# Kernel optimization log

Hardware: AMD Instinct MI355X
Metric: run time of the kernel (lower is better)

Reference implementation:

```python
import jax, jax.numpy as jnp
import numpy as np
import math

DIM = 512
MIN_THRES = -5.0
MAX_THRES = 7.0


def setup_inputs() -> dict:
    key = jax.random.key(0)
    k1, k2, k3, k4, k5 = jax.random.split(key, 5)
    s_len, batch, dim = 256, 256, DIM
    x = jax.random.normal(k1, (s_len, batch, dim), dtype=jnp.float32)
    # Linear(dim, dim, bias=False) weights, torch convention y = x @ W.T
    Wq = jax.random.normal(k2, (dim, dim), dtype=jnp.float32) * 0.02
    Wk = jax.random.normal(k3, (dim, dim), dtype=jnp.float32) * 0.02
    Wv = jax.random.normal(k4, (dim, dim), dtype=jnp.float32) * 0.02
    root_query = jax.random.normal(k5, (dim,), dtype=jnp.float32)
    return {"x": x, "Wq": Wq, "Wk": Wk, "Wv": Wv, "root_query": root_query}


def _matrix_tree(score):
    # score: [b, s, s]. Batched matrix-tree theorem marginals (lengths=None -> full length).
    b, s, _ = score.shape
    eye = jnp.eye(s, dtype=score.dtype)
    A = jnp.exp(score)                                  # exp(input)
    rd = jnp.exp(jnp.diagonal(score, axis1=1, axis2=2))  # exp(diag) root scores [b, s]
    L_off = A * (1.0 - eye)                              # mask diagonal
    colsum = L_off.sum(axis=1)                           # lap.sum(0): column sums [b, s]
    lap = -L_off + eye * colsum[:, None, :]              # -A_off + diag(colsum)
    lap = lap.at[:, 0, :].set(rd)                        # lap[0] = exp(diag(input))
    inv = jnp.linalg.inv(lap)                            # [b, s, s]
    inv_diag = jnp.diagonal(inv, axis1=1, axis2=2)       # [b, s]
    term1 = A * inv_diag[:, None, :]                     # factor[i,j] = inv_diag[j]
    term2 = A * jnp.swapaxes(inv, 1, 2)
    term1 = term1.at[:, :, 0].set(0.0)
    term2 = term2.at[:, 0, :].set(0.0)
    roots = rd * inv[:, :, 0]                            # diag(input).exp() * inv.T[0]
    return term1 - term2 + roots[:, :, None] * eye       # [b, s, s]


def reference(x, Wq, Wk, Wv, root_query):
    s_len, batch, dim = x.shape
    scale = math.sqrt(1.0 / dim)
    xt = jnp.swapaxes(x, 0, 1)                           # [b, s, d]
    q = jnp.einsum('bsd,ed->bse', xt, Wq)
    k = jnp.einsum('bsd,ed->bse', xt, Wk)
    v = jnp.einsum('bsd,ed->bse', xt, Wv)
    _score = jnp.einsum('bsd,btd->bst', q, k)            # [b, s, s]
    root = jnp.einsum('bsd,d->bs', k, root_query)        # [b, s]
    eye = jnp.eye(s_len, dtype=x.dtype)
    # Faithful to source: score[b] = _score[b]*eye + diag(root[b]) (off-diagonal zeroed)
    score = _score * eye + root[:, :, None] * eye
    score = jnp.clip(score * scale, MIN_THRES, MAX_THRES)
    edge_score = jnp.swapaxes(_matrix_tree(score), 1, 2)  # [b, s, s]
    return jnp.einsum('bst,btd->bsd', edge_score, v)
```

## Files before the change

kernel.cpp:

```cpp
#include <hip/hip_runtime.h>

typedef __bf16 v8bf __attribute__((ext_vector_type(8)));
typedef float f32x4 __attribute__((ext_vector_type(4)));
typedef unsigned short u16x8 __attribute__((ext_vector_type(8)));

#define SLEN 256
#define BATCH 256
#define DIM 512
#define SCALE 0.044194173824159216f

#define TS 64
#define LDX 520
#define LDB 72
#define KC 64

#define MFMA(a, b, c) __builtin_amdgcn_mfma_f32_16x16x32_bf16((a), (b), (c), 0, 0, 0)

__device__ __forceinline__ unsigned int f2bf(float f) {
  union { float f; unsigned int u; } v; v.f = f;
  unsigned int r = v.u + 0x7FFFu + ((v.u >> 16) & 1u);
  return r >> 16;
}
__device__ __forceinline__ float bf2f(unsigned short u) {
  union { unsigned int u; float f; } v; v.u = ((unsigned int)u) << 16;
  return v.f;
}
__device__ __forceinline__ v8bf ld8(const unsigned short* p) {
  u16x8 t = *reinterpret_cast<const u16x8*>(p);
  return __builtin_bit_cast(v8bf, t);
}
__device__ __forceinline__ void gload16(const unsigned short* g, unsigned short* l) {
  __builtin_amdgcn_global_load_lds(
      (const __attribute__((address_space(1))) unsigned int*)g,
      (__attribute__((address_space(3))) unsigned int*)l, 16, 0, 0);
}

__global__ __launch_bounds__(256) void zf(float4* __restrict__ p, int n4) {
  const int i = blockIdx.x * 256 + threadIdx.x;
  if (i < n4) {
    const float4 z = {0.f, 0.f, 0.f, 0.f};
    p[i] = z;
  }
}

__global__ __launch_bounds__(256) void prep_all(const float* __restrict__ X,
                                                const float* __restrict__ Wq,
                                                const float* __restrict__ Wk,
                                                const float* __restrict__ Wv,
                                                const float* __restrict__ rq,
                                                unsigned short* __restrict__ Xsb,
                                                unsigned short* __restrict__ Mt,
                                                unsigned short* __restrict__ Wvb,
                                                float* __restrict__ wkr) {
  __shared__ float As[32][33];
  __shared__ float Bs[32][33];
  const int blk = blockIdx.x;
  const int tid = threadIdx.x;

  if (blk >= 514) {
    const size_t base = (size_t)(blk - 514) * 16384;
#pragma unroll
    for (int j = 0; j < 8; ++j) {
      const float* s = X + base + (size_t)j * 2048 + tid * 8;
      const float4 a = *reinterpret_cast<const float4*>(s);
      const float4 b = *reinterpret_cast<const float4*>(s + 4);
      uint4 p;
      p.x = f2bf(a.x) | (f2bf(a.y) << 16);
      p.y = f2bf(a.z) | (f2bf(a.w) << 16);
      p.z = f2bf(b.x) | (f2bf(b.y) << 16);
      p.w = f2bf(b.z) | (f2bf(b.w) << 16);
      *reinterpret_cast<uint4*>(Xsb + base + (size_t)j * 2048 + tid * 8) = p;
    }
  } else if (blk < 256) {
    const int e0 = (blk & 15) * 32;
    const int d0 = (blk >> 4) * 32;
    const int tm = (tid & 15) * 2;
    const int tn = (tid >> 4) * 2;
    const int lf = tid >> 3;
    const int lc = (tid & 7) * 4;
    float a00 = 0.f, a01 = 0.f, a10 = 0.f, a11 = 0.f;
    for (int f0 = 0; f0 < DIM; f0 += 32) {
      __syncthreads();
      const float4 a = *reinterpret_cast<const float4*>(Wk + (size_t)(f0 + lf) * DIM + e0 + lc);
      const float4 b = *reinterpret_cast<const float4*>(Wq + (size_t)(f0 + lf) * DIM + d0 + lc);
      As[lf][lc] = a.x; As[lf][lc + 1] = a.y; As[lf][lc + 2] = a.z; As[lf][lc + 3] = a.w;
      Bs[lf][lc] = b.x; Bs[lf][lc + 1] = b.y; Bs[lf][lc + 2] = b.z; Bs[lf][lc + 3] = b.w;
      __syncthreads();
#pragma unroll
      for (int k = 0; k < 32; ++k) {
        const float x0 = As[k][tm], x1 = As[k][tm + 1];
        const float y0 = Bs[k][tn], y1 = Bs[k][tn + 1];
        a00 += x0 * y0; a01 += x0 * y1; a10 += x1 * y0; a11 += x1 * y1;
      }
    }
    Mt[(size_t)(e0 + tm) * DIM + d0 + tn] = (unsigned short)f2bf(a00);
    Mt[(size_t)(e0 + tm) * DIM + d0 + tn + 1] = (unsigned short)f2bf(a01);
    Mt[(size_t)(e0 + tm + 1) * DIM + d0 + tn] = (unsigned short)f2bf(a10);
    Mt[(size_t)(e0 + tm + 1) * DIM + d0 + tn + 1] = (unsigned short)f2bf(a11);
  } else if (blk < 512) {
    const int idx = ((blk - 256) * 256 + tid) * 4;
    const float4 v = *reinterpret_cast<const float4*>(Wv + idx);
    uint2 p;
    p.x = f2bf(v.x) | (f2bf(v.y) << 16);
    p.y = f2bf(v.z) | (f2bf(v.w) << 16);
    *reinterpret_cast<uint2*>(Wvb + idx) = p;
  } else {
    float* rqs = &As[0][0];
    rqs[tid] = rq[tid];
    rqs[tid + 256] = rq[tid + 256];
    __syncthreads();
    const int d = (blk - 512) * 256 + tid;
    float s = 0.f;
#pragma unroll 8
    for (int f = 0; f < DIM; ++f) s += Wk[(size_t)f * DIM + d] * rqs[f];
    wkr[d] = s;
  }
}


#define GEMM_PROLOGUE()                                                         \
  f32x4 acc[8][4] = {};                                                         \
  STG(0); STG(1); STG(2);

#define GEMM_MAIN_LOOP()                                                        \
  for (int t = 0; t < 16; ++t) {                                                \
    if (t <= 13) { asm volatile("s_waitcnt vmcnt(8)" ::: "memory"); }           \
    else if (t == 14) { asm volatile("s_waitcnt vmcnt(4)" ::: "memory"); }      \
    else { asm volatile("s_waitcnt vmcnt(0)" ::: "memory"); }                   \
    __builtin_amdgcn_s_barrier();                                               \
    __builtin_amdgcn_sched_barrier(0);                                          \
    if (t + 3 < 16) { STG(t + 3); }                                             \
    __builtin_amdgcn_sched_barrier(0);                                          \
    const unsigned short* la = lds + (t & 3) * 16384;                           \
    const unsigned short* lb2 = la + 8192;                                      \
    v8bf a[8], bbf[4];                                                          \
    _Pragma("unroll")                                                           \
    for (int m = 0; m < 8; ++m)                                                 \
      a[m] = ld8(la + (wr * 128 + m * 16 + c) * 32 + grd);                      \
    _Pragma("unroll")                                                           \
    for (int n = 0; n < 4; ++n)                                                 \
      bbf[n] = ld8(lb2 + (wc * 64 + n * 16 + c) * 32 + grd);                    \
    __builtin_amdgcn_s_setprio(1);                                              \
    _Pragma("unroll")                                                           \
    for (int m = 0; m < 8; ++m)                                                 \
      _Pragma("unroll")                                                         \
      for (int n = 0; n < 4; ++n) acc[m][n] = MFMA(a[m], bbf[n], acc[m][n]);    \
    __builtin_amdgcn_s_setprio(0);                                              \
  }

#define STG(tt) {                                                               \
    const int kc_ = (tt) * 32;                                                  \
    unsigned short* lb_ = lw + ((tt) & 3) * 16384;                              \
    gload16(sAp + kc_, lb_);                                                    \
    gload16(sAp + kc_ + sA2, lb_ + 4096);                                       \
    gload16(sBp + kc_, lb_ + 8192);                                             \
    gload16(sBp + kc_ + sB2, lb_ + 12288); }

__global__ __launch_bounds__(512, 2) void gemm1_dp(const unsigned short* __restrict__ Xsb,
                                                   const unsigned short* __restrict__ Mt,
                                                   const float* __restrict__ wkr,
                                                   float* __restrict__ rdpart) {
  __shared__ unsigned short lds[65536];
  const int tid = threadIdx.x;
  const int lane = tid & 63, w = tid >> 6;
  const int wr = w >> 2, wc = w & 3;
  const int c = lane & 15, g = lane >> 4;
  const int grd = ((g ^ ((c >> 1) & 3))) * 8;

  const int work = (blockIdx.x & 7) * 64 + (blockIdx.x >> 3);
  const int rt = work >> 1, ct = work & 1;
  const int j0 = rt * 256, e0 = ct * 256;

  const int rA = tid >> 2;
  const int gl = (tid & 3) ^ ((rA >> 1) & 3);
  const unsigned short* sAp = Xsb + ((size_t)rA * BATCH + rt) * DIM + gl * 8;
  const unsigned short* sBp = Mt + (size_t)(e0 + rA) * DIM + gl * 8;
  const size_t sA2 = (size_t)128 * BATCH * DIM;
  const size_t sB2 = (size_t)128 * DIM;
  unsigned short* lw = lds + (w << 9);

  GEMM_PROLOGUE()
  GEMM_MAIN_LOOP()

  __syncthreads();
  float* red = (float*)lds;
  float wkrl[4];
#pragma unroll
  for (int n = 0; n < 4; ++n) wkrl[n] = wkr[e0 + wc * 64 + n * 16 + c];
#pragma unroll
  for (int m = 0; m < 8; ++m) {
#pragma unroll
    for (int i = 0; i < 4; ++i) {
      const int rl = wr * 128 + m * 16 + 4 * g + i;
      const unsigned short* xrow = Xsb + ((size_t)rl * BATCH + rt) * DIM + e0 + wc * 64 + c;
      float val = 0.f;
#pragma unroll
      for (int n = 0; n < 4; ++n)
        val += (acc[m][n][i] + wkrl[n]) * bf2f(xrow[n * 16]);
      val += __shfl_xor(val, 1); val += __shfl_xor(val, 2);
      val += __shfl_xor(val, 4); val += __shfl_xor(val, 8);
      if (c == 0) red[wc * 256 + rl] = val;
    }
  }
  __syncthreads();
  if (tid < 256) {
    const float s = red[tid] + red[256 + tid] + red[512 + tid] + red[768 + tid];
    rdpart[(size_t)ct * 65536 + j0 + tid] = s;
  }
}

__global__ __launch_bounds__(512, 2) void gemm2_f(const unsigned short* __restrict__ Xsb,
                                                  const unsigned short* __restrict__ Wvb,
                                                  const float* __restrict__ rdpart,
                                                  float* __restrict__ out) {
  __shared__ unsigned short lds[65536];
  __shared__ float rdl[256];
  __shared__ float wsum[4];
  const int tid = threadIdx.x;
  const int lane = tid & 63, w = tid >> 6;
  const int wr = w >> 2, wc = w & 3;
  const int c = lane & 15, g = lane >> 4;
  const int grd = ((g ^ ((c >> 1) & 3))) * 8;

  const int work = (blockIdx.x & 7) * 64 + (blockIdx.x >> 3);
  const int rt = work >> 1, ct = work & 1;
  const int j0 = rt * 256, e0 = ct * 256;
  const int b = rt;

  if (tid < 256) {
    float v = (rdpart[(size_t)b * SLEN + tid] + rdpart[65536 + (size_t)b * SLEN + tid]) * SCALE;
    v = fminf(fmaxf(v, -5.0f), 7.0f);
    const float r = expf(v);
    rdl[tid] = r;
    float t = r;
    t += __shfl_xor(t, 1);  t += __shfl_xor(t, 2);  t += __shfl_xor(t, 4);
    t += __shfl_xor(t, 8);  t += __shfl_xor(t, 16); t += __shfl_xor(t, 32);
    if ((tid & 63) == 0) wsum[tid >> 6] = t;
  }
  __syncthreads();

  const int rA = tid >> 2;
  const int gl = (tid & 3) ^ ((rA >> 1) & 3);
  const unsigned short* sAp = Xsb + ((size_t)rA * BATCH + b) * DIM + gl * 8;
  const unsigned short* sBp = Wvb + (size_t)(e0 + rA) * DIM + gl * 8;
  const size_t sA2 = (size_t)128 * BATCH * DIM;
  const size_t sB2 = (size_t)128 * DIM;
  unsigned short* lw = lds + (w << 9);

  GEMM_PROLOGUE()
  GEMM_MAIN_LOOP()

  float vsp[4] = {0.f, 0.f, 0.f, 0.f}, vwp[4] = {0.f, 0.f, 0.f, 0.f};
#pragma unroll
  for (int m = 0; m < 8; ++m) {
#pragma unroll
    for (int i = 0; i < 4; ++i) {
      const int rl = wr * 128 + m * 16 + 4 * g + i;
      const float rr = rdl[rl];
#pragma unroll
      for (int n = 0; n < 4; ++n) {
        vsp[n] += acc[m][n][i];
        vwp[n] += rr * acc[m][n][i];
      }
    }
  }
#pragma unroll
  for (int n = 0; n < 4; ++n) {
    vsp[n] += __shfl_xor(vsp[n], 16); vsp[n] += __shfl_xor(vsp[n], 32);
    vwp[n] += __shfl_xor(vwp[n], 16); vwp[n] += __shfl_xor(vwp[n], 32);
  }
  __syncthreads();
  float* red = (float*)lds;
  if (g == 0) {
#pragma unroll
    for (int n = 0; n < 4; ++n) {
      red[(w * 4 + n) * 16 + c] = vsp[n];
      red[512 + (w * 4 + n) * 16 + c] = vwp[n];
    }
  }
  __syncthreads();
  const float Rb = wsum[0] + wsum[1] + wsum[2] + wsum[3];
  const float invR = 1.0f / Rb;
  const float gam = invR * 0.00390625f;
  const int wo = w ^ 4;
  float vsf[4], vwf[4];
#pragma unroll
  for (int n = 0; n < 4; ++n) {
    vsf[n] = red[(w * 4 + n) * 16 + c] + red[(wo * 4 + n) * 16 + c];
    vwf[n] = red[512 + (w * 4 + n) * 16 + c] + red[512 + (wo * 4 + n) * 16 + c];
  }
#pragma unroll
  for (int m = 0; m < 8; ++m) {
#pragma unroll
    for (int i = 0; i < 4; ++i) {
      const int rl = wr * 128 + m * 16 + 4 * g + i;
      const float tt = rdl[rl] * invR;
      const float al = tt - 0.00390625f;
      const float be = (1.0f - tt) * 0.00390625f;
      float* orow = out + (size_t)(j0 + rl) * DIM + e0 + wc * 64 + c;
#pragma unroll
      for (int n = 0; n < 4; ++n)
        orow[n * 16] = al * acc[m][n][i] + be * vsf[n] + gam * vwf[n];
    }
  }
}

__global__ __launch_bounds__(256) void prep_mt(const float* __restrict__ Wq,
                                               const float* __restrict__ Wk,
                                               unsigned short* __restrict__ Mt) {
  __shared__ float As[32][33];
  __shared__ float Bs[32][33];
  const int e0 = (blockIdx.x & 15) * 32;
  const int d0 = (blockIdx.x >> 4) * 32;
  const int tid = threadIdx.x;
  const int tm = (tid & 15) * 2;
  const int tn = (tid >> 4) * 2;
  const int lf = tid >> 3;
  const int lc = (tid & 7) * 4;
  float a00 = 0.f, a01 = 0.f, a10 = 0.f, a11 = 0.f;
  for (int f0 = 0; f0 < DIM; f0 += 32) {
    __syncthreads();
    const float4 a = *reinterpret_cast<const float4*>(Wk + (size_t)(f0 + lf) * DIM + e0 + lc);
    const float4 b = *reinterpret_cast<const float4*>(Wq + (size_t)(f0 + lf) * DIM + d0 + lc);
    As[lf][lc] = a.x; As[lf][lc + 1] = a.y; As[lf][lc + 2] = a.z; As[lf][lc + 3] = a.w;
    Bs[lf][lc] = b.x; Bs[lf][lc + 1] = b.y; Bs[lf][lc + 2] = b.z; Bs[lf][lc + 3] = b.w;
    __syncthreads();
#pragma unroll
    for (int k = 0; k < 32; ++k) {
      const float x0 = As[k][tm], x1 = As[k][tm + 1];
      const float y0 = Bs[k][tn], y1 = Bs[k][tn + 1];
      a00 += x0 * y0; a01 += x0 * y1; a10 += x1 * y0; a11 += x1 * y1;
    }
  }
  Mt[(size_t)(e0 + tm) * DIM + d0 + tn] = (unsigned short)f2bf(a00);
  Mt[(size_t)(e0 + tm) * DIM + d0 + tn + 1] = (unsigned short)f2bf(a01);
  Mt[(size_t)(e0 + tm + 1) * DIM + d0 + tn] = (unsigned short)f2bf(a10);
  Mt[(size_t)(e0 + tm + 1) * DIM + d0 + tn + 1] = (unsigned short)f2bf(a11);
}

__global__ __launch_bounds__(256) void conv_wv(const float* __restrict__ Wv,
                                               unsigned short* __restrict__ Wvb) {
  const int idx = (blockIdx.x * 256 + threadIdx.x) * 4;
  const float4 v = *reinterpret_cast<const float4*>(Wv + idx);
  uint2 p;
  p.x = f2bf(v.x) | (f2bf(v.y) << 16);
  p.y = f2bf(v.z) | (f2bf(v.w) << 16);
  *reinterpret_cast<uint2*>(Wvb + idx) = p;
}

__global__ __launch_bounds__(256) void wkr_k2(const float* __restrict__ Wk,
                                              const float* __restrict__ rq,
                                              float* __restrict__ wkr) {
  __shared__ float rqs[DIM];
  const int tid = threadIdx.x;
  rqs[tid] = rq[tid];
  rqs[tid + 256] = rq[tid + 256];
  __syncthreads();
  const int d = blockIdx.x * 256 + tid;
  float s = 0.f;
#pragma unroll 8
  for (int f = 0; f < DIM; ++f) s += Wk[(size_t)f * DIM + d] * rqs[f];
  wkr[d] = s;
}

__global__ __launch_bounds__(256, 2) void pass1_fb(
    const float* __restrict__ X, const unsigned short* __restrict__ Mt,
    const float* __restrict__ wkr, float* __restrict__ rd_out,
    float* __restrict__ Rsum, float* __restrict__ xsum, float* __restrict__ xw) {
  __shared__ __align__(16) unsigned short Xs[TS * LDX];
  __shared__ __align__(16) unsigned short Bsh[64 * LDB];
  __shared__ float wkrs[DIM];
  __shared__ float dacc[TS];
  __shared__ float rds[TS];
  const int tid = threadIdx.x;
  const int b = blockIdx.x & 255;
  const int s0 = (blockIdx.x >> 8) * TS;
  const int lane = tid & 63;
  const int wave = tid >> 6;
  const int wr = wave >> 1, wc = wave & 1;
  const int g = lane >> 4, c = lane & 15;
#pragma unroll 4
  for (int r = 0; r < TS; ++r) {
    const float2 v = *reinterpret_cast<const float2*>(
        X + ((size_t)(s0 + r) * BATCH + b) * DIM + tid * 2);
    Xs[r * LDX + tid * 2] = (unsigned short)f2bf(v.x);
    Xs[r * LDX + tid * 2 + 1] = (unsigned short)f2bf(v.y);
  }
  wkrs[tid] = wkr[tid];
  wkrs[tid + 256] = wkr[tid + 256];
  if (tid < TS) dacc[tid] = 0.f;
  float dp0[4] = {0.f, 0.f, 0.f, 0.f};
  float dp1[4] = {0.f, 0.f, 0.f, 0.f};
  for (int et = 0; et < 8; ++et) {
    const int e0 = et * 64;
    f32x4 acc00 = {0.f,0.f,0.f,0.f}, acc01 = {0.f,0.f,0.f,0.f};
    f32x4 acc10 = {0.f,0.f,0.f,0.f}, acc11 = {0.f,0.f,0.f,0.f};
    for (int kc0 = 0; kc0 < DIM; kc0 += KC) {
      __syncthreads();
      {
        const int e = tid >> 2;
        const int kq = (tid & 3) * 16;
        const uint4* src = reinterpret_cast<const uint4*>(Mt + (size_t)(e0 + e) * DIM + kc0 + kq);
        const uint4 w0 = src[0];
        const uint4 w1 = src[1];
        *reinterpret_cast<uint4*>(&Bsh[e * LDB + kq]) = w0;
        *reinterpret_cast<uint4*>(&Bsh[e * LDB + kq + 8]) = w1;
      }
      __syncthreads();
#pragma unroll
      for (int ks = 0; ks < KC; ks += 32) {
        const int ka = kc0 + ks + 8 * g;
        const int kb = ks + 8 * g;
        const v8bf fa0 = ld8(&Xs[(32 * wr + c) * LDX + ka]);
        const v8bf fa1 = ld8(&Xs[(32 * wr + 16 + c) * LDX + ka]);
        const v8bf fb0 = ld8(&Bsh[(32 * wc + c) * LDB + kb]);
        const v8bf fb1 = ld8(&Bsh[(32 * wc + 16 + c) * LDB + kb]);
        acc00 = MFMA(fa0, fb0, acc00);
        acc01 = MFMA(fa0, fb1, acc01);
        acc10 = MFMA(fa1, fb0, acc10);
        acc11 = MFMA(fa1, fb1, acc11);
      }
    }
#pragma unroll
    for (int i = 0; i < 4; ++i) {
      const int r0 = 32 * wr + 4 * g + i;
      const int ec0 = e0 + 32 * wc + c;
      const float w0 = wkrs[ec0], w1 = wkrs[ec0 + 16];
      dp0[i] += (acc00[i] + w0) * bf2f(Xs[r0 * LDX + ec0]) +
                (acc01[i] + w1) * bf2f(Xs[r0 * LDX + ec0 + 16]);
      dp1[i] += (acc10[i] + w0) * bf2f(Xs[(r0 + 16) * LDX + ec0]) +
                (acc11[i] + w1) * bf2f(Xs[(r0 + 16) * LDX + ec0 + 16]);
    }
  }
#pragma unroll
  for (int i = 0; i < 4; ++i) {
    float v0 = dp0[i], v1 = dp1[i];
    v0 += __shfl_xor(v0, 1); v0 += __shfl_xor(v0, 2);
    v0 += __shfl_xor(v0, 4); v0 += __shfl_xor(v0, 8);
    v1 += __shfl_xor(v1, 1); v1 += __shfl_xor(v1, 2);
    v1 += __shfl_xor(v1, 4); v1 += __shfl_xor(v1, 8);
    if (c == 0) {
      atomicAdd(&dacc[32 * wr + 4 * g + i], v0);
      atomicAdd(&dacc[32 * wr + 16 + 4 * g + i], v1);
    }
  }
  __syncthreads();
  if (tid < TS) {
    float sc = dacc[tid] * SCALE;
    sc = fminf(fmaxf(sc, -5.0f), 7.0f);
    const float r = expf(sc);
    rds[tid] = r;
    rd_out[(size_t)b * SLEN + s0 + tid] = r;
    float t = r;
    t += __shfl_xor(t, 1); t += __shfl_xor(t, 2); t += __shfl_xor(t, 4);
    t += __shfl_xor(t, 8); t += __shfl_xor(t, 16); t += __shfl_xor(t, 32);
    if (tid == 0) atomicAdd(&Rsum[b], t);
  }
  __syncthreads();
#pragma unroll
  for (int dd = 0; dd < 2; ++dd) {
    const int d = tid + dd * 256;
    float s1 = 0.f, s2 = 0.f;
    for (int r = 0; r < TS; ++r) {
      const float xv = bf2f(Xs[r * LDX + d]);
      s1 += xv;
      s2 += rds[r] * xv;
    }
    atomicAdd(&xsum[(size_t)b * DIM + d], s1);
    atomicAdd(&xw[(size_t)b * DIM + d], s2);
  }
}

__global__ __launch_bounds__(256, 2) void pass2_fb(
    const float* __restrict__ X, const unsigned short* __restrict__ Wvb,
    const float* __restrict__ rd, const float* __restrict__ Rsum,
    const float* __restrict__ xsum, const float* __restrict__ xw,
    float* __restrict__ out) {
  __shared__ __align__(16) unsigned short Zs[TS * LDX];
  __shared__ __align__(16) unsigned short Bsh[64 * LDB];
  __shared__ float xss[DIM];
  __shared__ float xws[DIM];
  __shared__ float rds[TS];
  const int tid = threadIdx.x;
  const int b = blockIdx.x & 255;
  const int s0 = (blockIdx.x >> 8) * TS;
  const int lane = tid & 63;
  const int wave = tid >> 6;
  const int wr = wave >> 1, wc = wave & 1;
  const int g = lane >> 4, c = lane & 15;
  xss[tid] = xsum[(size_t)b * DIM + tid];
  xss[tid + 256] = xsum[(size_t)b * DIM + tid + 256];
  xws[tid] = xw[(size_t)b * DIM + tid];
  xws[tid + 256] = xw[(size_t)b * DIM + tid + 256];
  if (tid < TS) rds[tid] = rd[(size_t)b * SLEN + s0 + tid];
  const float Rb = Rsum[b];
  const float invR = 1.0f / Rb;
  const float gam = invR * (1.0f / 256.0f);
  __syncthreads();
#pragma unroll 4
  for (int r = 0; r < TS; ++r) {
    const float rv = rds[r];
    const float al = rv * invR - (1.0f / 256.0f);
    const float be = (1.0f - rv * invR) * (1.0f / 256.0f);
    const float2 v = *reinterpret_cast<const float2*>(
        X + ((size_t)(s0 + r) * BATCH + b) * DIM + tid * 2);
    const int d0 = tid * 2;
    Zs[r * LDX + d0] = (unsigned short)f2bf(al * v.x + be * xss[d0] + gam * xws[d0]);
    Zs[r * LDX + d0 + 1] = (unsigned short)f2bf(al * v.y + be * xss[d0 + 1] + gam * xws[d0 + 1]);
  }
  const size_t outbase = ((size_t)b * SLEN + s0) * DIM;
  for (int et = 0; et < 8; ++et) {
    const int e0 = et * 64;
    f32x4 acc00 = {0.f,0.f,0.f,0.f}, acc01 = {0.f,0.f,0.f,0.f};
    f32x4 acc10 = {0.f,0.f,0.f,0.f}, acc11 = {0.f,0.f,0.f,0.f};
    for (int kc0 = 0; kc0 < DIM; kc0 += KC) {
      __syncthreads();
      {
        const int e = tid >> 2;
        const int kq = (tid & 3) * 16;
        const uint4* src = reinterpret_cast<const uint4*>(Wvb + (size_t)(e0 + e) * DIM + kc0 + kq);
        const uint4 w0 = src[0];
        const uint4 w1 = src[1];
        *reinterpret_cast<uint4*>(&Bsh[e * LDB + kq]) = w0;
        *reinterpret_cast<uint4*>(&Bsh[e * LDB + kq + 8]) = w1;
      }
      __syncthreads();
#pragma unroll
      for (int ks = 0; ks < KC; ks += 32) {
        const int ka = kc0 + ks + 8 * g;
        const int kb = ks + 8 * g;
        const v8bf fa0 = ld8(&Zs[(32 * wr + c) * LDX + ka]);
        const v8bf fa1 = ld8(&Zs[(32 * wr + 16 + c) * LDX + ka]);
        const v8bf fb0 = ld8(&Bsh[(32 * wc + c) * LDB + kb]);
        const v8bf fb1 = ld8(&Bsh[(32 * wc + 16 + c) * LDB + kb]);
        acc00 = MFMA(fa0, fb0, acc00);
        acc01 = MFMA(fa0, fb1, acc01);
        acc10 = MFMA(fa1, fb0, acc10);
        acc11 = MFMA(fa1, fb1, acc11);
      }
    }
#pragma unroll
    for (int i = 0; i < 4; ++i) {
      const int r0 = 32 * wr + 4 * g + i;
      const int c0 = e0 + 32 * wc + c;
      out[outbase + (size_t)r0 * DIM + c0] = acc00[i];
      out[outbase + (size_t)r0 * DIM + c0 + 16] = acc01[i];
      out[outbase + (size_t)(r0 + 16) * DIM + c0] = acc10[i];
      out[outbase + (size_t)(r0 + 16) * DIM + c0 + 16] = acc11[i];
    }
  }
}

extern "C" void kernel_launch(void* const* d_in, const int* in_sizes, int n_in,
                              void* d_out, int out_size, void* d_ws, size_t ws_size,
                              hipStream_t stream) {
  (void)in_sizes; (void)n_in; (void)out_size;
  const float* X = (const float*)d_in[0];
  const float* Wq = (const float*)d_in[1];
  const float* Wk = (const float*)d_in[2];
  const float* Wv = (const float*)d_in[3];
  const float* rq = (const float*)d_in[4];
  float* out = (float*)d_out;
  char* ws = (char*)d_ws;

  unsigned short* Mt = (unsigned short*)(ws + 0);
  unsigned short* Wvb = (unsigned short*)(ws + 524288);

  const size_t NEED = 69206016;
  if (ws_size >= NEED) {
    float* wkr = (float*)(ws + 1048576);
    float* rdpart = (float*)(ws + 1052672);
    unsigned short* Xsb = (unsigned short*)(ws + 2097152);

    prep_all<<<dim3(2562), dim3(256), 0, stream>>>(X, Wq, Wk, Wv, rq, Xsb, Mt, Wvb, wkr);
    gemm1_dp<<<dim3(512), dim3(512), 0, stream>>>(Xsb, Mt, wkr, rdpart);
    gemm2_f<<<dim3(512), dim3(512), 0, stream>>>(Xsb, Wvb, rdpart, out);
  } else {
    float* rd = (float*)(ws + 1048576);
    float* wkr = (float*)(ws + 1310720);
    float* Rsum = (float*)(ws + 1312768);
    float* xsum = (float*)(ws + 1313792);
    float* xw = (float*)(ws + 1838080);
    zf<<<dim3(257), dim3(256), 0, stream>>>((float4*)(ws + 1310720), 65728);
    prep_mt<<<dim3(256), dim3(256), 0, stream>>>(Wq, Wk, Mt);
    conv_wv<<<dim3(256), dim3(256), 0, stream>>>(Wv, Wvb);
    wkr_k2<<<dim3(2), dim3(256), 0, stream>>>(Wk, rq, wkr);
    pass1_fb<<<dim3(1024), dim3(256), 0, stream>>>(X, Mt, wkr, rd, Rsum, xsum, xw);
    pass2_fb<<<dim3(1024), dim3(256), 0, stream>>>(X, Wvb, rd, Rsum, xsum, xw, out);
  }
}
```

Baseline: 181.4 us.

## Use full-width 256x512 tiles with 1024-thread blocks, 3-stage LDS pipeline

Both GEMM kernels now use 1024-thread blocks, each computing a 256x512 output tile instead of two 256x256 halves. The A tile (X rows) is loaded once per block rather than twice, and gemm1 finishes the root score (clamp, exp, per-batch sum) itself instead of writing two partial sums. The LDS pipeline drops from 4 stages with 3 in flight to 3 stages with 2 in flight, to fit the larger B tile. The grid halves to 256 blocks at one block per CU, which lowers occupancy and leaves less latency hiding.

```diff
diff --git a/kernel.cpp b/kernel.cpp
--- a/kernel.cpp
+++ b/kernel.cpp
@@ -118,20 +118,24 @@
 }
 
 
-#define GEMM_PROLOGUE()                                                         \
+#define STG2(tt) {                                                              \
+    const int kc_ = (tt) * 32;                                                  \
+    unsigned short* lb_ = lds + ((tt) % 3) * 24576 + (w << 9);                  \
+    gload16(sAp + kc_, lb_);                                                    \
+    gload16(sBp + kc_, lb_ + 8192);                                             \
+    gload16(sBp + kc_ + (size_t)256 * DIM, lb_ + 16384); }
+
+#define GEMM2_MAIN()                                                            \
   f32x4 acc[8][4] = {};                                                         \
-  STG(0); STG(1); STG(2);
-
-#define GEMM_MAIN_LOOP()                                                        \
+  STG2(0); STG2(1);                                                             \
   for (int t = 0; t < 16; ++t) {                                                \
-    if (t <= 13) { asm volatile("s_waitcnt vmcnt(8)" ::: "memory"); }           \
-    else if (t == 14) { asm volatile("s_waitcnt vmcnt(4)" ::: "memory"); }      \
+    if (t <= 14) { asm volatile("s_waitcnt vmcnt(3)" ::: "memory"); }           \
     else { asm volatile("s_waitcnt vmcnt(0)" ::: "memory"); }                   \
     __builtin_amdgcn_s_barrier();                                               \
     __builtin_amdgcn_sched_barrier(0);                                          \
-    if (t + 3 < 16) { STG(t + 3); }                                             \
+    if (t + 2 < 16) { STG2(t + 2); }                                            \
     __builtin_amdgcn_sched_barrier(0);                                          \
-    const unsigned short* la = lds + (t & 3) * 16384;                           \
+    const unsigned short* la = lds + (t % 3) * 24576;                           \
     const unsigned short* lb2 = la + 8192;                                      \
     v8bf a[8], bbf[4];                                                          \
     _Pragma("unroll")                                                           \
@@ -148,51 +152,39 @@
     __builtin_amdgcn_s_setprio(0);                                              \
   }
 
-#define STG(tt) {                                                               \
-    const int kc_ = (tt) * 32;                                                  \
-    unsigned short* lb_ = lw + ((tt) & 3) * 16384;                              \
-    gload16(sAp + kc_, lb_);                                                    \
-    gload16(sAp + kc_ + sA2, lb_ + 4096);                                       \
-    gload16(sBp + kc_, lb_ + 8192);                                             \
-    gload16(sBp + kc_ + sB2, lb_ + 12288); }
-
-__global__ __launch_bounds__(512, 2) void gemm1_dp(const unsigned short* __restrict__ Xsb,
-                                                   const unsigned short* __restrict__ Mt,
-                                                   const float* __restrict__ wkr,
-                                                   float* __restrict__ rdpart) {
-  __shared__ unsigned short lds[65536];
+__global__ __launch_bounds__(1024, 1) void gemm1_f2(const unsigned short* __restrict__ Xsb,
+                                                    const unsigned short* __restrict__ Mt,
+                                                    const float* __restrict__ wkr,
+                                                    float* __restrict__ rd,
+                                                    float* __restrict__ Rsum) {
+  __shared__ unsigned short lds[73728];
   const int tid = threadIdx.x;
   const int lane = tid & 63, w = tid >> 6;
-  const int wr = w >> 2, wc = w & 3;
+  const int wr = w >> 3, wc = w & 7;
   const int c = lane & 15, g = lane >> 4;
   const int grd = ((g ^ ((c >> 1) & 3))) * 8;
 
-  const int work = (blockIdx.x & 7) * 64 + (blockIdx.x >> 3);
-  const int rt = work >> 1, ct = work & 1;
-  const int j0 = rt * 256, e0 = ct * 256;
+  const int rt = (blockIdx.x & 7) * 32 + (blockIdx.x >> 3);
+  const int j0 = rt * 256;
 
   const int rA = tid >> 2;
   const int gl = (tid & 3) ^ ((rA >> 1) & 3);
   const unsigned short* sAp = Xsb + ((size_t)rA * BATCH + rt) * DIM + gl * 8;
-  const unsigned short* sBp = Mt + (size_t)(e0 + rA) * DIM + gl * 8;
-  const size_t sA2 = (size_t)128 * BATCH * DIM;
-  const size_t sB2 = (size_t)128 * DIM;
-  unsigned short* lw = lds + (w << 9);
-
-  GEMM_PROLOGUE()
-  GEMM_MAIN_LOOP()
+  const unsigned short* sBp = Mt + (size_t)rA * DIM + gl * 8;
+
+  GEMM2_MAIN()
 
   __syncthreads();
   float* red = (float*)lds;
   float wkrl[4];
 #pragma unroll
-  for (int n = 0; n < 4; ++n) wkrl[n] = wkr[e0 + wc * 64 + n * 16 + c];
+  for (int n = 0; n < 4; ++n) wkrl[n] = wkr[wc * 64 + n * 16 + c];
 #pragma unroll
   for (int m = 0; m < 8; ++m) {
 #pragma unroll
     for (int i = 0; i < 4; ++i) {
       const int rl = wr * 128 + m * 16 + 4 * g + i;
-      const unsigned short* xrow = Xsb + ((size_t)rl * BATCH + rt) * DIM + e0 + wc * 64 + c;
+      const unsigned short* xrow = Xsb + ((size_t)rl * BATCH + rt) * DIM + wc * 64 + c;
       float val = 0.f;
 #pragma unroll
       for (int n = 0; n < 4; ++n)
@@ -204,51 +196,51 @@
   }
   __syncthreads();
   if (tid < 256) {
-    const float s = red[tid] + red[256 + tid] + red[512 + tid] + red[768 + tid];
-    rdpart[(size_t)ct * 65536 + j0 + tid] = s;
-  }
-}
-
-__global__ __launch_bounds__(512, 2) void gemm2_f(const unsigned short* __restrict__ Xsb,
-                                                  const unsigned short* __restrict__ Wvb,
-                                                  const float* __restrict__ rdpart,
-                                                  float* __restrict__ out) {
-  __shared__ unsigned short lds[65536];
-  __shared__ float rdl[256];
-  __shared__ float wsum[4];
-  const int tid = threadIdx.x;
-  const int lane = tid & 63, w = tid >> 6;
-  const int wr = w >> 2, wc = w & 3;
-  const int c = lane & 15, g = lane >> 4;
-  const int grd = ((g ^ ((c >> 1) & 3))) * 8;
-
-  const int work = (blockIdx.x & 7) * 64 + (blockIdx.x >> 3);
-  const int rt = work >> 1, ct = work & 1;
-  const int j0 = rt * 256, e0 = ct * 256;
-  const int b = rt;
-
-  if (tid < 256) {
-    float v = (rdpart[(size_t)b * SLEN + tid] + rdpart[65536 + (size_t)b * SLEN + tid]) * SCALE;
-    v = fminf(fmaxf(v, -5.0f), 7.0f);
-    const float r = expf(v);
-    rdl[tid] = r;
+    float s = 0.f;
+#pragma unroll
+    for (int k = 0; k < 8; ++k) s += red[k * 256 + tid];
+    s *= SCALE;
+    s = fminf(fmaxf(s, -5.0f), 7.0f);
+    const float r = expf(s);
+    rd[(size_t)j0 + tid] = r;
     float t = r;
     t += __shfl_xor(t, 1);  t += __shfl_xor(t, 2);  t += __shfl_xor(t, 4);
     t += __shfl_xor(t, 8);  t += __shfl_xor(t, 16); t += __shfl_xor(t, 32);
-    if ((tid & 63) == 0) wsum[tid >> 6] = t;
-  }
-  __syncthreads();
+    if ((tid & 63) == 0) red[2048 + (tid >> 6)] = t;
+  }
+  __syncthreads();
+  if (tid == 0) Rsum[rt] = red[2048] + red[2049] + red[2050] + red[2051];
+}
+
+__global__ __launch_bounds__(1024, 1) void gemm2_f2(const unsigned short* __restrict__ Xsb,
+                                                    const unsigned short* __restrict__ Wvb,
+                                                    const float* __restrict__ rd,
+                                                    const float* __restrict__ Rsum,
+                                                    float* __restrict__ out) {
+  __shared__ unsigned short lds[73728];
+  const int tid = threadIdx.x;
+  const int lane = tid & 63, w = tid >> 6;
+  const int wr = w >> 3, wc = w & 7;
+  const int c = lane & 15, g = lane >> 4;
+  const int grd = ((g ^ ((c >> 1) & 3))) * 8;
+
+  const int rt = (blockIdx.x & 7) * 32 + (blockIdx.x >> 3);
+  const int j0 = rt * 256;
+
+  const float rme = (tid < 256) ? rd[(size_t)j0 + tid] : 0.f;
+  const float Rb = Rsum[rt];
 
   const int rA = tid >> 2;
   const int gl = (tid & 3) ^ ((rA >> 1) & 3);
-  const unsigned short* sAp = Xsb + ((size_t)rA * BATCH + b) * DIM + gl * 8;
-  const unsigned short* sBp = Wvb + (size_t)(e0 + rA) * DIM + gl * 8;
-  const size_t sA2 = (size_t)128 * BATCH * DIM;
-  const size_t sB2 = (size_t)128 * DIM;
-  unsigned short* lw = lds + (w << 9);
-
-  GEMM_PROLOGUE()
-  GEMM_MAIN_LOOP()
+  const unsigned short* sAp = Xsb + ((size_t)rA * BATCH + rt) * DIM + gl * 8;
+  const unsigned short* sBp = Wvb + (size_t)rA * DIM + gl * 8;
+
+  GEMM2_MAIN()
+
+  __syncthreads();
+  float* red = (float*)lds;
+  if (tid < 256) red[2048 + tid] = rme;
+  __syncthreads();
 
   float vsp[4] = {0.f, 0.f, 0.f, 0.f}, vwp[4] = {0.f, 0.f, 0.f, 0.f};
 #pragma unroll
@@ -256,7 +248,7 @@
 #pragma unroll
     for (int i = 0; i < 4; ++i) {
       const int rl = wr * 128 + m * 16 + 4 * g + i;
-      const float rr = rdl[rl];
+      const float rr = red[2048 + rl];
 #pragma unroll
       for (int n = 0; n < 4; ++n) {
         vsp[n] += acc[m][n][i];
@@ -270,34 +262,32 @@
     vwp[n] += __shfl_xor(vwp[n], 16); vwp[n] += __shfl_xor(vwp[n], 32);
   }
   __syncthreads();
-  float* red = (float*)lds;
   if (g == 0) {
 #pragma unroll
     for (int n = 0; n < 4; ++n) {
       red[(w * 4 + n) * 16 + c] = vsp[n];
-      red[512 + (w * 4 + n) * 16 + c] = vwp[n];
-    }
-  }
-  __syncthreads();
-  const float Rb = wsum[0] + wsum[1] + wsum[2] + wsum[3];
+      red[1024 + (w * 4 + n) * 16 + c] = vwp[n];
+    }
+  }
+  __syncthreads();
   const float invR = 1.0f / Rb;
   const float gam = invR * 0.00390625f;
-  const int wo = w ^ 4;
+  const int wo = w ^ 8;
   float vsf[4], vwf[4];
 #pragma unroll
   for (int n = 0; n < 4; ++n) {
     vsf[n] = red[(w * 4 + n) * 16 + c] + red[(wo * 4 + n) * 16 + c];
-    vwf[n] = red[512 + (w * 4 + n) * 16 + c] + red[512 + (wo * 4 + n) * 16 + c];
+    vwf[n] = red[1024 + (w * 4 + n) * 16 + c] + red[1024 + (wo * 4 + n) * 16 + c];
   }
 #pragma unroll
   for (int m = 0; m < 8; ++m) {
 #pragma unroll
     for (int i = 0; i < 4; ++i) {
       const int rl = wr * 128 + m * 16 + 4 * g + i;
-      const float tt = rdl[rl] * invR;
+      const float tt = red[2048 + rl] * invR;
       const float al = tt - 0.00390625f;
       const float be = (1.0f - tt) * 0.00390625f;
-      float* orow = out + (size_t)(j0 + rl) * DIM + e0 + wc * 64 + c;
+      float* orow = out + (size_t)(j0 + rl) * DIM + wc * 64 + c;
 #pragma unroll
       for (int n = 0; n < 4; ++n)
         orow[n * 16] = al * acc[m][n][i] + be * vsf[n] + gam * vwf[n];
@@ -569,12 +559,13 @@
   const size_t NEED = 69206016;
   if (ws_size >= NEED) {
     float* wkr = (float*)(ws + 1048576);
-    float* rdpart = (float*)(ws + 1052672);
+    float* rd = (float*)(ws + 1052672);
+    float* Rsum = (float*)(ws + 1314816);
     unsigned short* Xsb = (unsigned short*)(ws + 2097152);
 
     prep_all<<<dim3(2562), dim3(256), 0, stream>>>(X, Wq, Wk, Wv, rq, Xsb, Mt, Wvb, wkr);
-    gemm1_dp<<<dim3(512), dim3(512), 0, stream>>>(Xsb, Mt, wkr, rdpart);
-    gemm2_f<<<dim3(512), dim3(512), 0, stream>>>(Xsb, Wvb, rdpart, out);
+    gemm1_f2<<<dim3(256), dim3(1024), 0, stream>>>(Xsb, Mt, wkr, rd, Rsum);
+    gemm2_f2<<<dim3(256), dim3(1024), 0, stream>>>(Xsb, Wvb, rd, Rsum, out);
   } else {
     float* rd = (float*)(ws + 1048576);
     float* wkr = (float*)(ws + 1310720);
```

New measurement: 724.6 us. 3.99x slower.

## Fuse X fp32-to-bf16 conversion into first GEMM's A-operand load path

Applied to the files above, without the earlier changes.

Removes the separate bulk X conversion from the prep kernel. The first GEMM now loads fp32 X straight from global memory, converts it to bf16 in registers and writes it to LDS. Each block also writes its own column half of bf16 X to the workspace, which the second GEMM reads later. This saves a full extra read/write pass over X. The cost is a simpler two-stage register-staged pipeline in place of the deeper async global-to-LDS prefetch, and each row tile of fp32 X is read by two blocks.

```diff
diff --git a/kernel.cpp b/kernel.cpp
--- a/kernel.cpp
+++ b/kernel.cpp
@@ -43,35 +43,19 @@
   }
 }
 
-__global__ __launch_bounds__(256) void prep_all(const float* __restrict__ X,
-                                                const float* __restrict__ Wq,
-                                                const float* __restrict__ Wk,
-                                                const float* __restrict__ Wv,
-                                                const float* __restrict__ rq,
-                                                unsigned short* __restrict__ Xsb,
-                                                unsigned short* __restrict__ Mt,
-                                                unsigned short* __restrict__ Wvb,
-                                                float* __restrict__ wkr) {
+__global__ __launch_bounds__(256) void prep_small(const float* __restrict__ Wq,
+                                                  const float* __restrict__ Wk,
+                                                  const float* __restrict__ Wv,
+                                                  const float* __restrict__ rq,
+                                                  unsigned short* __restrict__ Mt,
+                                                  unsigned short* __restrict__ Wvb,
+                                                  float* __restrict__ wkr) {
   __shared__ float As[32][33];
   __shared__ float Bs[32][33];
   const int blk = blockIdx.x;
   const int tid = threadIdx.x;
 
-  if (blk >= 514) {
-    const size_t base = (size_t)(blk - 514) * 16384;
-#pragma unroll
-    for (int j = 0; j < 8; ++j) {
-      const float* s = X + base + (size_t)j * 2048 + tid * 8;
-      const float4 a = *reinterpret_cast<const float4*>(s);
-      const float4 b = *reinterpret_cast<const float4*>(s + 4);
-      uint4 p;
-      p.x = f2bf(a.x) | (f2bf(a.y) << 16);
-      p.y = f2bf(a.z) | (f2bf(a.w) << 16);
-      p.z = f2bf(b.x) | (f2bf(b.y) << 16);
-      p.w = f2bf(b.z) | (f2bf(b.w) << 16);
-      *reinterpret_cast<uint4*>(Xsb + base + (size_t)j * 2048 + tid * 8) = p;
-    }
-  } else if (blk < 256) {
+  if (blk < 256) {
     const int e0 = (blk & 15) * 32;
     const int d0 = (blk >> 4) * 32;
     const int tm = (tid & 15) * 2;
@@ -117,6 +101,123 @@
   }
 }
 
+__global__ __launch_bounds__(512, 2) void gemm1_x(const float* __restrict__ X,
+                                                  const unsigned short* __restrict__ Mt,
+                                                  const float* __restrict__ wkr,
+                                                  unsigned short* __restrict__ Xsb,
+                                                  float* __restrict__ rdpart) {
+  __shared__ unsigned short lds[32768];
+  const int tid = threadIdx.x;
+  const int lane = tid & 63, w = tid >> 6;
+  const int wr = w >> 2, wc = w & 3;
+  const int c = lane & 15, g = lane >> 4;
+  const int grd = ((g ^ ((c >> 1) & 3))) * 8;
+
+  const int work = (blockIdx.x & 7) * 64 + (blockIdx.x >> 3);
+  const int rt = work >> 1, ct = work & 1;
+  const int j0 = rt * 256, e0 = ct * 256;
+
+  const int rA = tid >> 1;
+  const int h = tid & 1;
+  const int sw = (rA >> 1) & 3;
+  const int q1 = (2 * h) ^ sw;
+  const int q2 = (2 * h + 1) ^ sw;
+  const float* xrowp = X + ((size_t)rA * BATCH + rt) * DIM;
+  unsigned short* xsrow = Xsb + ((size_t)rA * BATCH + rt) * DIM;
+
+  const int rB = tid >> 2;
+  const int glB = (tid & 3) ^ ((rB >> 1) & 3);
+  const unsigned short* sBp = Mt + (size_t)(e0 + rB) * DIM + glB * 8;
+
+#define LOADA1(t, va, vb, vc, vd) {                                             \
+    const int kc_ = (t) * 32;                                                   \
+    va = *reinterpret_cast<const float4*>(xrowp + kc_ + q1 * 8);                \
+    vb = *reinterpret_cast<const float4*>(xrowp + kc_ + q1 * 8 + 4);            \
+    vc = *reinterpret_cast<const float4*>(xrowp + kc_ + q2 * 8);                \
+    vd = *reinterpret_cast<const float4*>(xrowp + kc_ + q2 * 8 + 4); }
+
+#define WRITEA1(t, va, vb, vc, vd) {                                            \
+    const int kc_ = (t) * 32;                                                   \
+    unsigned short* lb_ = lds + ((t) & 1) * 16384;                              \
+    uint4 p1, p2;                                                               \
+    p1.x = f2bf(va.x) | (f2bf(va.y) << 16);                                     \
+    p1.y = f2bf(va.z) | (f2bf(va.w) << 16);                                     \
+    p1.z = f2bf(vb.x) | (f2bf(vb.y) << 16);                                     \
+    p1.w = f2bf(vb.z) | (f2bf(vb.w) << 16);                                     \
+    p2.x = f2bf(vc.x) | (f2bf(vc.y) << 16);                                     \
+    p2.y = f2bf(vc.z) | (f2bf(vc.w) << 16);                                     \
+    p2.z = f2bf(vd.x) | (f2bf(vd.y) << 16);                                     \
+    p2.w = f2bf(vd.z) | (f2bf(vd.w) << 16);                                     \
+    *reinterpret_cast<uint4*>(lb_ + rA * 32 + (2 * h) * 8) = p1;                \
+    *reinterpret_cast<uint4*>(lb_ + rA * 32 + (2 * h + 1) * 8) = p2;            \
+    if (((t) >> 3) == ct) {               \
+      *reinterpret_cast<uint4*>(xsrow + kc_ + q1 * 8) = p1;                     \
+      *reinterpret_cast<uint4*>(xsrow + kc_ + q2 * 8) = p2;                     \
+    } }
+
+#define GLOADB1(t) {                                                            \
+    const int kc_ = (t) * 32;                                                   \
+    unsigned short* lb_ = lds + ((t) & 1) * 16384 + 8192 + (w << 9);            \
+    gload16(sBp + kc_, lb_);                                                    \
+    gload16(sBp + kc_ + (size_t)128 * DIM, lb_ + 4096); }
+
+  f32x4 acc[8][4] = {};
+  {
+    float4 a0, a1, a2, a3;
+    LOADA1(0, a0, a1, a2, a3);
+    GLOADB1(0);
+    WRITEA1(0, a0, a1, a2, a3);
+  }
+  __syncthreads();
+  for (int t = 0; t < 16; ++t) {
+    const int cur = t & 1;
+    float4 n0, n1, n2, n3;
+    if (t < 15) {
+      LOADA1(t + 1, n0, n1, n2, n3);
+      GLOADB1(t + 1);
+    }
+    const unsigned short* la = lds + cur * 16384;
+    const unsigned short* lb2 = la + 8192;
+    v8bf a[8], bbf[4];
+#pragma unroll
+    for (int m = 0; m < 8; ++m) a[m] = ld8(la + (wr * 128 + m * 16 + c) * 32 + grd);
+#pragma unroll
+    for (int n = 0; n < 4; ++n) bbf[n] = ld8(lb2 + (wc * 64 + n * 16 + c) * 32 + grd);
+    __builtin_amdgcn_s_setprio(1);
+#pragma unroll
+    for (int m = 0; m < 8; ++m)
+#pragma unroll
+      for (int n = 0; n < 4; ++n) acc[m][n] = MFMA(a[m], bbf[n], acc[m][n]);
+    __builtin_amdgcn_s_setprio(0);
+    if (t < 15) WRITEA1(t + 1, n0, n1, n2, n3);
+    __syncthreads();
+  }
+
+  float* red = (float*)lds;
+  float wkrl[4];
+#pragma unroll
+  for (int n = 0; n < 4; ++n) wkrl[n] = wkr[e0 + wc * 64 + n * 16 + c];
+#pragma unroll
+  for (int m = 0; m < 8; ++m) {
+#pragma unroll
+    for (int i = 0; i < 4; ++i) {
+      const int rl = wr * 128 + m * 16 + 4 * g + i;
+      const unsigned short* xrow = Xsb + ((size_t)rl * BATCH + rt) * DIM + e0 + wc * 64 + c;
+      float val = 0.f;
+#pragma unroll
+      for (int n = 0; n < 4; ++n)
+        val += (acc[m][n][i] + wkrl[n]) * bf2f(xrow[n * 16]);
+      val += __shfl_xor(val, 1); val += __shfl_xor(val, 2);
+      val += __shfl_xor(val, 4); val += __shfl_xor(val, 8);
+      if (c == 0) red[wc * 256 + rl] = val;
+    }
+  }
+  __syncthreads();
+  if (tid < 256) {
+    const float s = red[tid] + red[256 + tid] + red[512 + tid] + red[768 + tid];
+    rdpart[(size_t)ct * 65536 + j0 + tid] = s;
+  }
+}
 
 #define GEMM_PROLOGUE()                                                         \
   f32x4 acc[8][4] = {};                                                         \
@@ -131,7 +232,7 @@
     __builtin_amdgcn_sched_barrier(0);                                          \
     if (t + 3 < 16) { STG(t + 3); }                                             \
     __builtin_amdgcn_sched_barrier(0);                                          \
-    const unsigned short* la = lds + (t & 3) * 16384;                           \
+    const unsigned short* la = ldsp + (t & 3) * 16384;                          \
     const unsigned short* lb2 = la + 8192;                                      \
     v8bf a[8], bbf[4];                                                          \
     _Pragma("unroll")                                                           \
@@ -156,64 +257,11 @@
     gload16(sBp + kc_, lb_ + 8192);                                             \
     gload16(sBp + kc_ + sB2, lb_ + 12288); }
 
-__global__ __launch_bounds__(512, 2) void gemm1_dp(const unsigned short* __restrict__ Xsb,
-                                                   const unsigned short* __restrict__ Mt,
-                                                   const float* __restrict__ wkr,
-                                                   float* __restrict__ rdpart) {
-  __shared__ unsigned short lds[65536];
-  const int tid = threadIdx.x;
-  const int lane = tid & 63, w = tid >> 6;
-  const int wr = w >> 2, wc = w & 3;
-  const int c = lane & 15, g = lane >> 4;
-  const int grd = ((g ^ ((c >> 1) & 3))) * 8;
-
-  const int work = (blockIdx.x & 7) * 64 + (blockIdx.x >> 3);
-  const int rt = work >> 1, ct = work & 1;
-  const int j0 = rt * 256, e0 = ct * 256;
-
-  const int rA = tid >> 2;
-  const int gl = (tid & 3) ^ ((rA >> 1) & 3);
-  const unsigned short* sAp = Xsb + ((size_t)rA * BATCH + rt) * DIM + gl * 8;
-  const unsigned short* sBp = Mt + (size_t)(e0 + rA) * DIM + gl * 8;
-  const size_t sA2 = (size_t)128 * BATCH * DIM;
-  const size_t sB2 = (size_t)128 * DIM;
-  unsigned short* lw = lds + (w << 9);
-
-  GEMM_PROLOGUE()
-  GEMM_MAIN_LOOP()
-
-  __syncthreads();
-  float* red = (float*)lds;
-  float wkrl[4];
-#pragma unroll
-  for (int n = 0; n < 4; ++n) wkrl[n] = wkr[e0 + wc * 64 + n * 16 + c];
-#pragma unroll
-  for (int m = 0; m < 8; ++m) {
-#pragma unroll
-    for (int i = 0; i < 4; ++i) {
-      const int rl = wr * 128 + m * 16 + 4 * g + i;
-      const unsigned short* xrow = Xsb + ((size_t)rl * BATCH + rt) * DIM + e0 + wc * 64 + c;
-      float val = 0.f;
-#pragma unroll
-      for (int n = 0; n < 4; ++n)
-        val += (acc[m][n][i] + wkrl[n]) * bf2f(xrow[n * 16]);
-      val += __shfl_xor(val, 1); val += __shfl_xor(val, 2);
-      val += __shfl_xor(val, 4); val += __shfl_xor(val, 8);
-      if (c == 0) red[wc * 256 + rl] = val;
-    }
-  }
-  __syncthreads();
-  if (tid < 256) {
-    const float s = red[tid] + red[256 + tid] + red[512 + tid] + red[768 + tid];
-    rdpart[(size_t)ct * 65536 + j0 + tid] = s;
-  }
-}
-
 __global__ __launch_bounds__(512, 2) void gemm2_f(const unsigned short* __restrict__ Xsb,
                                                   const unsigned short* __restrict__ Wvb,
                                                   const float* __restrict__ rdpart,
                                                   float* __restrict__ out) {
-  __shared__ unsigned short lds[65536];
+  __shared__ unsigned short ldsp[65536];
   __shared__ float rdl[256];
   __shared__ float wsum[4];
   const int tid = threadIdx.x;
@@ -242,10 +290,12 @@
   const int rA = tid >> 2;
   const int gl = (tid & 3) ^ ((rA >> 1) & 3);
   const unsigned short* sAp = Xsb + ((size_t)rA * BATCH + b) * DIM + gl * 8;
-  const unsigned short* sBp = Wvb + (size_t)(e0 + rA) * DIM + gl * 8;
+  const unsigned short* sBp = Wvb + (size_t)rA * DIM + gl * 8;
   const size_t sA2 = (size_t)128 * BATCH * DIM;
   const size_t sB2 = (size_t)128 * DIM;
-  unsigned short* lw = lds + (w << 9);
+  unsigned short* lw = ldsp + (w << 9);
+  const unsigned short* sBp2 = sBp + (size_t)e0 * DIM;
+  sBp = sBp2;
 
   GEMM_PROLOGUE()
   GEMM_MAIN_LOOP()
@@ -270,7 +320,7 @@
     vwp[n] += __shfl_xor(vwp[n], 16); vwp[n] += __shfl_xor(vwp[n], 32);
   }
   __syncthreads();
-  float* red = (float*)lds;
+  float* red = (float*)ldsp;
   if (g == 0) {
 #pragma unroll
     for (int n = 0; n < 4; ++n) {
@@ -572,8 +622,8 @@
     float* rdpart = (float*)(ws + 1052672);
     unsigned short* Xsb = (unsigned short*)(ws + 2097152);
 
-    prep_all<<<dim3(2562), dim3(256), 0, stream>>>(X, Wq, Wk, Wv, rq, Xsb, Mt, Wvb, wkr);
-    gemm1_dp<<<dim3(512), dim3(512), 0, stream>>>(Xsb, Mt, wkr, rdpart);
+    prep_small<<<dim3(514), dim3(256), 0, stream>>>(Wq, Wk, Wv, rq, Mt, Wvb, wkr);
+    gemm1_x<<<dim3(512), dim3(512), 0, stream>>>(X, Mt, wkr, Xsb, rdpart);
     gemm2_f<<<dim3(512), dim3(512), 0, stream>>>(Xsb, Wvb, rdpart, out);
   } else {
     float* rd = (float*)(ws + 1048576);
```

Result: slower. 187.4 us (+3.3%).
